# Performance work log

Hardware: AMD Instinct MI355X
Metric: run time of the kernel (lower is better)

## Reference

```python
import jax, jax.numpy as jnp
import numpy as np

D = 300  # feature dim hardcoded in the layer
L = 50   # headline length (e = ones(50))
B = 16384


def setup_inputs() -> dict:
    key = jax.random.key(0)
    ks = jax.random.split(key, 7)
    s = 0.05  # keras initializations.get('normal') uses scale=0.05
    return {
        "Y": jax.random.normal(ks[0], (B, D, L), dtype=jnp.float32),
        "h_n": jax.random.normal(ks[1], (B, D), dtype=jnp.float32),
        "W_y": s * jax.random.normal(ks[2], (D, D), dtype=jnp.float32),
        "W_h": s * jax.random.normal(ks[3], (D, D), dtype=jnp.float32),
        "W_p": s * jax.random.normal(ks[4], (D, D), dtype=jnp.float32),
        "W_x": s * jax.random.normal(ks[5], (D, D), dtype=jnp.float32),
        "w": s * jax.random.normal(ks[6], (D,), dtype=jnp.float32),
    }


def reference(Y, h_n, W_y, W_h, W_p, W_x, w):
    # M = tanh(W_y Y + (W_h h_n) e^T)   -> [B, D, L]
    Wh_h = jnp.einsum('de,be->bd', W_h, h_n)            # [B, D]
    M = jnp.tanh(jnp.einsum('de,bel->bdl', W_y, Y) + Wh_h[:, :, None])
    # alpha = softmax(w^T M) over headline positions    -> [B, L]
    alpha = jax.nn.softmax(jnp.einsum('d,bdl->bl', w, M), axis=-1)
    # r = Y alpha^T                                      -> [B, D]
    r = jnp.einsum('bdl,bl->bd', Y, alpha)
    # h* = tanh(W_p r + W_x h_n)                         -> [B, D]
    h = jnp.tanh(jnp.einsum('de,be->bd', W_p, r) + jnp.einsum('de,be->bd', W_x, h_n))
    return h
```

## Files before the change

kernel.cpp:

```cpp
#include <hip/hip_runtime.h>
#include <hip/hip_bf16.h>

typedef __attribute__((ext_vector_type(8))) short bf16x8;
typedef __attribute__((ext_vector_type(4))) float f32x4;
typedef unsigned short u16;
typedef unsigned int u32;

__device__ __forceinline__ u16 f2bf(float f){
    u32 u; __builtin_memcpy(&u,&f,4);
    u = (u + 0x7FFFu + ((u>>16)&1u)) >> 16;
    return (u16)u;
}
__device__ __forceinline__ float bf2f(u16 h){
    u32 u = ((u32)h)<<16; float f; __builtin_memcpy(&f,&u,4); return f;
}
__device__ __forceinline__ u32 pkbf(float a, float b){
    __hip_bfloat162 h = __float22bfloat162_rn(float2{a,b});
    u32 r; __builtin_memcpy(&r,&h,4); return r;
}
__device__ __forceinline__ float fast_tanh(float x){
    float e = __builtin_amdgcn_exp2f(x * 2.8853900817779268f);
    return 1.f - 2.f*__builtin_amdgcn_rcpf(e + 1.f);
}
__device__ __forceinline__ float wval(const float* W, int d, int e){
    return (d<300 && e<300) ? W[d*300+e] : 0.f;
}

__global__ void k_prep(const float* __restrict__ Wy, const float* __restrict__ Wh,
                       const float* __restrict__ Wp, const float* __restrict__ Wx,
                       const float* __restrict__ w,
                       u16* __restrict__ wy_swz, u16* __restrict__ wh_swz,
                       u16* __restrict__ wpx_swz, float* __restrict__ w_pad)
{
    int gid = blockIdx.x*256 + threadIdx.x;
    if (gid < 320) w_pad[gid] = (gid < 300) ? w[gid] : 0.f;
    u16* dst; const float* A; const float* Bm = nullptr; int t, nks;
    if (gid < 12800)      { dst = wy_swz;  t = gid;        nks = 10; A = Wy; }
    else if (gid < 25600) { dst = wh_swz;  t = gid-12800;  nks = 10; A = Wh; }
    else                  { dst = wpx_swz; t = gid-25600;  nks = 20; A = Wp; Bm = Wx; }
    int ks   = (t/64) % nks;
    int tile = t/(nks*64);
    int lane = t & 63;
    int d  = tile*16 + (lane & 15);
    int kb = ks*32 + (lane>>4)*8;
    u32 pk[4];
    #pragma unroll
    for (int jj=0; jj<4; jj++){
        int k0 = kb + 2*jj, k1 = k0 + 1;
        float v0, v1;
        if (Bm){ v0 = (k0 < 320) ? wval(A,d,k0) : wval(Bm,d,k0-320);
                 v1 = (k1 < 320) ? wval(A,d,k1) : wval(Bm,d,k1-320); }
        else   { v0 = wval(A,d,k0); v1 = wval(A,d,k1); }
        pk[jj] = (u32)f2bf(v0) | ((u32)f2bf(v1) << 16);
    }
    uint4 u; u.x = pk[0]; u.y = pk[1]; u.z = pk[2]; u.w = pk[3];
    ((uint4*)dst)[t] = u;
}

__global__ __launch_bounds__(256,3) void k_whh(const float* __restrict__ hn,
        const u16* __restrict__ wh_swz, u16* __restrict__ whh)
{
    __shared__ __align__(16) u16 A[64*328];
    int tid = threadIdx.x;
    int rb = blockIdx.x >> 1, half = blockIdx.x & 1;
    int m0 = rb*64;
    for (int i = tid; i < 9600; i += 256){
        int r = i/150, c = (i%150)*2;
        float2 v = *(const float2*)(hn + (size_t)(m0+r)*300 + c);
        *(u32*)&A[r*328 + c] = pkbf(v.x, v.y);
    }
    for (int i = tid; i < 64*14; i += 256){ int r = i/14, c = 300 + (i%14)*2; *(u32*)&A[r*328+c] = 0; }
    __syncthreads();
    int w = tid>>6, lane = tid&63, lo = lane&15, hi = lane>>4;
    f32x4 acc[10];
    #pragma unroll
    for (int t=0; t<10; t++) acc[t] = (f32x4){0.f,0.f,0.f,0.f};
    const bf16x8* wsz = (const bf16x8*)wh_swz;
    for (int ks=0; ks<10; ks++){
        bf16x8 aF = *(const bf16x8*)&A[(w*16+lo)*328 + ks*32 + hi*8];
        #pragma unroll
        for (int t=0; t<10; t++){
            int nt = half*10 + t;
            bf16x8 bF = wsz[(nt*10+ks)*64 + lane];
            acc[t] = __builtin_amdgcn_mfma_f32_16x16x32_bf16(aF, bF, acc[t], 0,0,0);
        }
    }
    #pragma unroll
    for (int t=0; t<10; t++)
      #pragma unroll
      for (int rg=0; rg<4; rg++){
        int m = m0 + w*16 + hi*4 + rg;
        whh[(size_t)m*320 + (half*10+t)*16 + lo] = f2bf(acc[t][rg]);
      }
}

__global__ __launch_bounds__(1024) void k_attn(const float* __restrict__ Y,
        const u16* __restrict__ whh, const u16* __restrict__ wy_swz,
        const float* __restrict__ w_pad, u16* __restrict__ r_out)
{
    __shared__ __align__(16) u16 Ylds[50*328];
    __shared__ float whh_s[320];
    __shared__ float w_s[320];
    __shared__ float s_red[8][64];
    __shared__ float alpha_s[64];

    const int tid = threadIdx.x;
    const int wv = tid>>6, lane = tid&63, lo = lane&15, hi = lane>>4;
    const int wd = wv>>1, wc = wv&1;
    const int hi16 = hi*16;
    const int b = blockIdx.x;
    char* Yb8 = (char*)Ylds;
    const float C2L = 2.8853900817779268f;

    int rb_[2];
    { int r0 = (2*wc)*16 + lo;   if (r0>=50) r0-=48; rb_[0]=r0*656;
      int r1 = (2*wc+1)*16 + lo; if (r1>=50) r1-=48; rb_[1]=r1*656; }

    for (int i = tid; i < 320; i += 1024) w_s[i] = w_pad[i];
    for (int i = tid; i < 700; i += 1024){
        int row = i/14, c2 = 150 + i%14;
        *(u32*)(Yb8 + row*656 + c2*4) = 0;
    }
    for (int i = tid; i < 160; i += 1024){
        u32 z = *(const u32*)&whh[(size_t)b*320 + 2*i];
        whh_s[2*i]   = bf2f((u16)(z & 0xffff));
        whh_s[2*i+1] = bf2f((u16)(z >> 16));
    }
    {
        const float* gb_ = Y + (size_t)b*15000;
        #pragma unroll
        for (int it=0; it<4; it++){
            int t = tid + it*1024;
            if (t < 3750){
                int e2 = t/25, l2 = t%25;
                const float* p_ = gb_ + e2*100 + 2*l2;
                float2 sA = *(const float2*)p_;
                float2 sB = *(const float2*)(p_ + 50);
                *(u32*)(Yb8 + (2*l2)*656   + e2*4) = pkbf(sA.x, sB.x);
                *(u32*)(Yb8 + (2*l2+1)*656 + e2*4) = pkbf(sA.y, sB.y);
            }
        }
    }
    __syncthreads();

    const bf16x8* wyf = (const bf16x8*)wy_swz;
    float sp[2] = {0.f,0.f};
    float swd = 0.f;
#define GEMM_BODY(NT)                                                          \
    {                                                                          \
        f32x4 acc[NT][2];                                                      \
        _Pragma("unroll") for (int q=0;q<NT;q++){                              \
            acc[q][0]=(f32x4){0.f,0.f,0.f,0.f};                                \
            acc[q][1]=(f32x4){0.f,0.f,0.f,0.f}; }                              \
        bf16x8 A0[NT], A1[NT], B0[2], B1[2];                                   \
        _Pragma("unroll") for (int q=0;q<NT;q++)                               \
            A0[q] = wyf[((wd+8*q)*10)*64 + lane];                              \
        B0[0] = *(const bf16x8*)(Yb8 + rb_[0] + hi16);                         \
        B0[1] = *(const bf16x8*)(Yb8 + rb_[1] + hi16);                         \
        _Pragma("unroll 1")                                                    \
        for (int kk=0; kk<5; kk++){                                            \
            int k1 = 2*kk+1, k2 = (2*kk+2<10)?(2*kk+2):0;                      \
            _Pragma("unroll") for (int q=0;q<NT;q++)                           \
                A1[q] = wyf[((wd+8*q)*10 + k1)*64 + lane];                     \
            B1[0] = *(const bf16x8*)(Yb8 + rb_[0] + k1*64 + hi16);             \
            B1[1] = *(const bf16x8*)(Yb8 + rb_[1] + k1*64 + hi16);             \
            _Pragma("unroll") for (int q=0;q<NT;q++){                          \
                acc[q][0] = __builtin_amdgcn_mfma_f32_16x16x32_bf16(A0[q],B0[0],acc[q][0],0,0,0); \
                acc[q][1] = __builtin_amdgcn_mfma_f32_16x16x32_bf16(A0[q],B0[1],acc[q][1],0,0,0); } \
            _Pragma("unroll") for (int q=0;q<NT;q++)                           \
                A0[q] = wyf[((wd+8*q)*10 + k2)*64 + lane];                     \
            B0[0] = *(const bf16x8*)(Yb8 + rb_[0] + k2*64 + hi16);             \
            B0[1] = *(const bf16x8*)(Yb8 + rb_[1] + k2*64 + hi16);             \
            _Pragma("unroll") for (int q=0;q<NT;q++){                          \
                acc[q][0] = __builtin_amdgcn_mfma_f32_16x16x32_bf16(A1[q],B1[0],acc[q][0],0,0,0); \
                acc[q][1] = __builtin_amdgcn_mfma_f32_16x16x32_bf16(A1[q],B1[1],acc[q][1],0,0,0); } \
        }                                                                      \
        _Pragma("unroll") for (int q=0;q<NT;q++)                               \
            _Pragma("unroll") for (int rg=0;rg<4;rg++){                        \
                int d = (wd+8*q)*16 + hi*4 + rg;                               \
                float wh = whh_s[d], wd_ = w_s[d];                             \
                float whc = wh*C2L, wd2n = -2.f*wd_;                           \
                swd += wd_;                                                    \
                _Pragma("unroll") for (int c=0;c<2;c++){                       \
                    float targ = __builtin_fmaf(acc[q][c][rg], C2L, whc);      \
                    float e2x  = __builtin_amdgcn_exp2f(targ);                 \
                    float rc   = __builtin_amdgcn_rcpf(e2x + 1.f);             \
                    sp[c] = __builtin_fmaf(wd2n, rc, sp[c]);                   \
                }                                                              \
            }                                                                  \
    }
    if (wd < 3) { GEMM_BODY(3) } else { GEMM_BODY(2) }
#undef GEMM_BODY
    #pragma unroll
    for (int c=0;c<2;c++){
        sp[c] += swd;
        sp[c] += __shfl_xor(sp[c], 16);
        sp[c] += __shfl_xor(sp[c], 32);
    }
    if (lane < 16){
        s_red[wd][(2*wc+0)*16 + lane] = sp[0];
        s_red[wd][(2*wc+1)*16 + lane] = sp[1];
    }
    __syncthreads();

    if (wv == 0){
        float sv = -1e30f;
        if (lane < 50){
            sv = 0.f;
            #pragma unroll
            for (int k=0;k<8;k++) sv += s_red[k][lane];
        }
        float mx = sv;
        #pragma unroll
        for (int off=32; off; off>>=1) mx = fmaxf(mx, __shfl_xor(mx, off));
        float pv = (lane < 50) ? __builtin_amdgcn_exp2f((sv - mx)*1.4426950408889634f) : 0.f;
        float sm = pv;
        #pragma unroll
        for (int off=32; off; off>>=1) sm += __shfl_xor(sm, off);
        alpha_s[lane] = pv * __builtin_amdgcn_rcpf(sm);
    }
    __syncthreads();

    if (tid < 160){
        float r0 = 0.f, r1 = 0.f;
        if (tid < 150){
            #pragma unroll 10
            for (int l=0; l<50; l++){
                u32 z = *(const u32*)(Yb8 + l*656 + tid*4);
                float a_ = alpha_s[l];
                r0 = __builtin_fmaf(a_, bf2f((u16)(z & 0xffff)), r0);
                r1 = __builtin_fmaf(a_, bf2f((u16)(z >> 16)),   r1);
            }
        }
        *(u32*)&r_out[(size_t)b*320 + 2*tid] = pkbf(r0, r1);
    }
}

__global__ __launch_bounds__(256,3) void k_out(const u16* __restrict__ r_in,
        const float* __restrict__ hn, const u16* __restrict__ wpx_swz,
        float* __restrict__ out)
{
    __shared__ __align__(16) u16 A[32*648];
    int tid = threadIdx.x;
    int m0 = blockIdx.x*32;
    for (int i = tid; i < 32*40; i += 256){
        int r = i/40, c8 = (i%40)*8;
        uint4 v = *(const uint4*)&r_in[(size_t)(m0+r)*320 + c8];
        *(uint4*)&A[r*648 + c8] = v;
    }
    for (int i = tid; i < 32*150; i += 256){
        int r = i/150, c = (i%150)*2;
        float2 v = *(const float2*)(hn + (size_t)(m0+r)*300 + c);
        *(u32*)&A[r*648 + 320 + c] = pkbf(v.x, v.y);
    }
    for (int i = tid; i < 32*14; i += 256){ int r = i/14, c = 620 + (i%14)*2; *(u32*)&A[r*648+c] = 0; }
    __syncthreads();
    int w = tid>>6, lane = tid&63, lo = lane&15, hi = lane>>4;
    int wm = w & 1, wn = w >> 1;
    f32x4 acc[10];
    #pragma unroll
    for (int t=0; t<10; t++) acc[t] = (f32x4){0.f,0.f,0.f,0.f};
    const bf16x8* wsz = (const bf16x8*)wpx_swz;
    for (int ks=0; ks<20; ks++){
        bf16x8 aF = *(const bf16x8*)&A[(wm*16+lo)*648 + ks*32 + hi*8];
        #pragma unroll
        for (int t=0; t<10; t++){
            int nt = wn*10 + t;
            bf16x8 bF = wsz[(nt*20+ks)*64 + lane];
            acc[t] = __builtin_amdgcn_mfma_f32_16x16x32_bf16(aF, bF, acc[t], 0,0,0);
        }
    }
    #pragma unroll
    for (int t=0; t<10; t++){
        int n = (wn*10+t)*16 + lo;
        if (n < 300){
            #pragma unroll
            for (int rg=0; rg<4; rg++){
                int m = m0 + wm*16 + hi*4 + rg;
                out[(size_t)m*300 + n] = fast_tanh(acc[t][rg]);
            }
        }
    }
}

extern "C" void kernel_launch(void* const* d_in, const int* in_sizes, int n_in,
                              void* d_out, int out_size, void* d_ws, size_t ws_size,
                              hipStream_t stream)
{
    const float* Y  = (const float*)d_in[0];
    const float* hn = (const float*)d_in[1];
    const float* Wy = (const float*)d_in[2];
    const float* Wh = (const float*)d_in[3];
    const float* Wp = (const float*)d_in[4];
    const float* Wx = (const float*)d_in[5];
    const float* w  = (const float*)d_in[6];
    int B = in_sizes[1] / 300;

    char* ws = (char*)d_ws;
    u16*   wy_swz  = (u16*)(ws + 0);
    u16*   wh_swz  = (u16*)(ws + 204800);
    u16*   wpx_swz = (u16*)(ws + 409600);
    float* w_pad   = (float*)(ws + 819200);
    u16*   whh     = (u16*)(ws + 820480);
    u16*   r_ws    = (u16*)(ws + 820480 + (size_t)B*640);

    k_prep<<<200, 256, 0, stream>>>(Wy, Wh, Wp, Wx, w, wy_swz, wh_swz, wpx_swz, w_pad);
    k_whh <<<(B/64)*2, 256, 0, stream>>>(hn, wh_swz, whh);
    k_attn<<<B, 1024, 0, stream>>>(Y, whh, wy_swz, w_pad, r_ws);
    k_out <<<B/32, 256, 0, stream>>>(r_ws, hn, wpx_swz, (float*)d_out);
}
```

Measured before the change: 485.6 us.

## Process two batch rows per attention block to reuse W_y fragments

Each k_attn block now handles two batch elements, stacking their Y tiles into one 100-column LDS buffer (stride reduced to 624 bytes). The column tiles are split 4/3 across wave pairs, so each W_y fragment loaded from global is reused across up to four MFMA column tiles instead of two. This halves the grid size and W_y fetch traffic per sample. In exchange it needs about 70KB of dynamic LDS, which may lower blocks per CU and makes the work uneven between wave pairs.

```diff
diff --git a/kernel.cpp b/kernel.cpp
--- a/kernel.cpp
+++ b/kernel.cpp
@@ -94,121 +94,146 @@
       }
 }
 
+#define YSTR 624
+#define OFF_SRED  62432
+#define OFF_ALPHA (62432+3584)
+#define OFF_WHH   (62432+3584+512)
+#define OFF_WS    (62432+3584+512+2560)
+#define DYN_LDS   70400
+
 __global__ __launch_bounds__(1024) void k_attn(const float* __restrict__ Y,
         const u16* __restrict__ whh, const u16* __restrict__ wy_swz,
         const float* __restrict__ w_pad, u16* __restrict__ r_out)
 {
-    __shared__ __align__(16) u16 Ylds[50*328];
-    __shared__ float whh_s[320];
-    __shared__ float w_s[320];
-    __shared__ float s_red[8][64];
-    __shared__ float alpha_s[64];
+    extern __shared__ __align__(16) char smem[];
+    char*  Yb8     = smem;
+    float (*s_red)[112] = (float(*)[112])(smem + OFF_SRED);
+    float (*alpha_s)[64]= (float(*)[64]) (smem + OFF_ALPHA);
+    float (*whh_s)[320] = (float(*)[320])(smem + OFF_WHH);
+    float* w_s          = (float*)       (smem + OFF_WS);
 
     const int tid = threadIdx.x;
     const int wv = tid>>6, lane = tid&63, lo = lane&15, hi = lane>>4;
     const int wd = wv>>1, wc = wv&1;
     const int hi16 = hi*16;
-    const int b = blockIdx.x;
-    char* Yb8 = (char*)Ylds;
+    const int b0 = blockIdx.x*2;
     const float C2L = 2.8853900817779268f;
 
-    int rb_[2];
-    { int r0 = (2*wc)*16 + lo;   if (r0>=50) r0-=48; rb_[0]=r0*656;
-      int r1 = (2*wc+1)*16 + lo; if (r1>=50) r1-=48; rb_[1]=r1*656; }
+    const int NCT = wc ? 3 : 4;
+    const int CB  = wc ? 4 : 0;
+    int rb_[4];
+    #pragma unroll
+    for (int c=0;c<4;c++){
+        int row = (CB + (c<NCT?c:0))*16 + lo;
+        if (row >= 100) row -= 48;
+        rb_[c] = row*YSTR;
+    }
 
     for (int i = tid; i < 320; i += 1024) w_s[i] = w_pad[i];
-    for (int i = tid; i < 700; i += 1024){
-        int row = i/14, c2 = 150 + i%14;
-        *(u32*)(Yb8 + row*656 + c2*4) = 0;
-    }
-    for (int i = tid; i < 160; i += 1024){
-        u32 z = *(const u32*)&whh[(size_t)b*320 + 2*i];
-        whh_s[2*i]   = bf2f((u16)(z & 0xffff));
-        whh_s[2*i+1] = bf2f((u16)(z >> 16));
+    for (int i = tid; i < 608; i += 1024){
+        if (i < 600){ int row = i/6, c2 = 150 + i%6;
+                      *(u32*)(Yb8 + row*YSTR + c2*4) = 0; }
+        else        { *(u32*)(Yb8 + 62400 + (i-600)*4) = 0; }
+    }
+    for (int i = tid; i < 320; i += 1024){
+        int bb = i/160, k = i%160;
+        u32 z = *(const u32*)&whh[(size_t)(b0+bb)*320 + 2*k];
+        whh_s[bb][2*k]   = bf2f((u16)(z & 0xffff));
+        whh_s[bb][2*k+1] = bf2f((u16)(z >> 16));
     }
     {
-        const float* gb_ = Y + (size_t)b*15000;
-        #pragma unroll
-        for (int it=0; it<4; it++){
+        const float* gb_ = Y + (size_t)b0*15000;
+        #pragma unroll
+        for (int it=0; it<8; it++){
             int t = tid + it*1024;
-            if (t < 3750){
-                int e2 = t/25, l2 = t%25;
-                const float* p_ = gb_ + e2*100 + 2*l2;
+            if (t < 7500){
+                int bb = t/3750, tt = t%3750;
+                int e2 = tt/25, l2 = tt%25;
+                const float* p_ = gb_ + bb*15000 + e2*100 + 2*l2;
                 float2 sA = *(const float2*)p_;
                 float2 sB = *(const float2*)(p_ + 50);
-                *(u32*)(Yb8 + (2*l2)*656   + e2*4) = pkbf(sA.x, sB.x);
-                *(u32*)(Yb8 + (2*l2+1)*656 + e2*4) = pkbf(sA.y, sB.y);
+                int r0 = bb*50 + 2*l2;
+                *(u32*)(Yb8 + r0*YSTR        + e2*4) = pkbf(sA.x, sB.x);
+                *(u32*)(Yb8 + (r0+1)*YSTR    + e2*4) = pkbf(sA.y, sB.y);
             }
         }
     }
     __syncthreads();
 
     const bf16x8* wyf = (const bf16x8*)wy_swz;
-    float sp[2] = {0.f,0.f};
+    float sp[4] = {0.f,0.f,0.f,0.f};
     float swd = 0.f;
 #define GEMM_BODY(NT)                                                          \
     {                                                                          \
-        f32x4 acc[NT][2];                                                      \
-        _Pragma("unroll") for (int q=0;q<NT;q++){                              \
-            acc[q][0]=(f32x4){0.f,0.f,0.f,0.f};                                \
-            acc[q][1]=(f32x4){0.f,0.f,0.f,0.f}; }                              \
-        bf16x8 A0[NT], A1[NT], B0[2], B1[2];                                   \
+        f32x4 acc[NT][4];                                                      \
+        _Pragma("unroll") for (int q=0;q<NT;q++)                               \
+            _Pragma("unroll") for (int c=0;c<4;c++)                            \
+                acc[q][c] = (f32x4){0.f,0.f,0.f,0.f};                          \
+        bf16x8 A0[NT], A1[NT], B[4];                                           \
         _Pragma("unroll") for (int q=0;q<NT;q++)                               \
             A0[q] = wyf[((wd+8*q)*10)*64 + lane];                              \
-        B0[0] = *(const bf16x8*)(Yb8 + rb_[0] + hi16);                         \
-        B0[1] = *(const bf16x8*)(Yb8 + rb_[1] + hi16);                         \
         _Pragma("unroll 1")                                                    \
         for (int kk=0; kk<5; kk++){                                            \
-            int k1 = 2*kk+1, k2 = (2*kk+2<10)?(2*kk+2):0;                      \
+            int k0 = 2*kk, k1 = 2*kk+1, k2 = (2*kk+2<10)?(2*kk+2):0;           \
             _Pragma("unroll") for (int q=0;q<NT;q++)                           \
                 A1[q] = wyf[((wd+8*q)*10 + k1)*64 + lane];                     \
-            B1[0] = *(const bf16x8*)(Yb8 + rb_[0] + k1*64 + hi16);             \
-            B1[1] = *(const bf16x8*)(Yb8 + rb_[1] + k1*64 + hi16);             \
-            _Pragma("unroll") for (int q=0;q<NT;q++){                          \
-                acc[q][0] = __builtin_amdgcn_mfma_f32_16x16x32_bf16(A0[q],B0[0],acc[q][0],0,0,0); \
-                acc[q][1] = __builtin_amdgcn_mfma_f32_16x16x32_bf16(A0[q],B0[1],acc[q][1],0,0,0); } \
+            _Pragma("unroll") for (int c=0;c<4;c++)                            \
+                if (c < NCT) B[c] = *(const bf16x8*)(Yb8 + rb_[c] + k0*64 + hi16); \
+            _Pragma("unroll") for (int q=0;q<NT;q++)                           \
+                _Pragma("unroll") for (int c=0;c<4;c++)                        \
+                    if (c < NCT)                                               \
+                        acc[q][c] = __builtin_amdgcn_mfma_f32_16x16x32_bf16(   \
+                            A0[q], B[c], acc[q][c], 0,0,0);                    \
             _Pragma("unroll") for (int q=0;q<NT;q++)                           \
                 A0[q] = wyf[((wd+8*q)*10 + k2)*64 + lane];                     \
-            B0[0] = *(const bf16x8*)(Yb8 + rb_[0] + k2*64 + hi16);             \
-            B0[1] = *(const bf16x8*)(Yb8 + rb_[1] + k2*64 + hi16);             \
-            _Pragma("unroll") for (int q=0;q<NT;q++){                          \
-                acc[q][0] = __builtin_amdgcn_mfma_f32_16x16x32_bf16(A1[q],B1[0],acc[q][0],0,0,0); \
-                acc[q][1] = __builtin_amdgcn_mfma_f32_16x16x32_bf16(A1[q],B1[1],acc[q][1],0,0,0); } \
+            _Pragma("unroll") for (int c=0;c<4;c++)                            \
+                if (c < NCT) B[c] = *(const bf16x8*)(Yb8 + rb_[c] + k1*64 + hi16); \
+            _Pragma("unroll") for (int q=0;q<NT;q++)                           \
+                _Pragma("unroll") for (int c=0;c<4;c++)                        \
+                    if (c < NCT)                                               \
+                        acc[q][c] = __builtin_amdgcn_mfma_f32_16x16x32_bf16(   \
+                            A1[q], B[c], acc[q][c], 0,0,0);                    \
         }                                                                      \
         _Pragma("unroll") for (int q=0;q<NT;q++)                               \
             _Pragma("unroll") for (int rg=0;rg<4;rg++){                        \
                 int d = (wd+8*q)*16 + hi*4 + rg;                               \
-                float wh = whh_s[d], wd_ = w_s[d];                             \
-                float whc = wh*C2L, wd2n = -2.f*wd_;                           \
+                float wh0 = whh_s[0][d], wh1 = whh_s[1][d], wd_ = w_s[d];      \
+                float wd2n = -2.f*wd_;                                         \
                 swd += wd_;                                                    \
-                _Pragma("unroll") for (int c=0;c<2;c++){                       \
-                    float targ = __builtin_fmaf(acc[q][c][rg], C2L, whc);      \
-                    float e2x  = __builtin_amdgcn_exp2f(targ);                 \
-                    float rc   = __builtin_amdgcn_rcpf(e2x + 1.f);             \
-                    sp[c] = __builtin_fmaf(wd2n, rc, sp[c]);                   \
+                _Pragma("unroll") for (int c=0;c<4;c++){                       \
+                    if (c < NCT){                                              \
+                        int col = (CB+c)*16 + lo;                              \
+                        float wh = (col < 50) ? wh0 : wh1;                     \
+                        float targ = (acc[q][c][rg] + wh) * C2L;               \
+                        float e2x  = __builtin_amdgcn_exp2f(targ);             \
+                        float rc   = __builtin_amdgcn_rcpf(e2x + 1.f);         \
+                        sp[c] = __builtin_fmaf(wd2n, rc, sp[c]);               \
+                    }                                                          \
                 }                                                              \
             }                                                                  \
     }
     if (wd < 3) { GEMM_BODY(3) } else { GEMM_BODY(2) }
 #undef GEMM_BODY
     #pragma unroll
-    for (int c=0;c<2;c++){
+    for (int c=0;c<4;c++){
         sp[c] += swd;
         sp[c] += __shfl_xor(sp[c], 16);
         sp[c] += __shfl_xor(sp[c], 32);
     }
     if (lane < 16){
-        s_red[wd][(2*wc+0)*16 + lane] = sp[0];
-        s_red[wd][(2*wc+1)*16 + lane] = sp[1];
-    }
-    __syncthreads();
-
-    if (wv == 0){
+        #pragma unroll
+        for (int c=0;c<4;c++)
+            if (c < NCT) s_red[wd][(CB+c)*16 + lane] = sp[c];
+    }
+    __syncthreads();
+
+    if (wv < 2){
+        int bb = wv;
         float sv = -1e30f;
         if (lane < 50){
             sv = 0.f;
             #pragma unroll
-            for (int k=0;k<8;k++) sv += s_red[k][lane];
+            for (int k=0;k<8;k++) sv += s_red[k][bb*50 + lane];
         }
         float mx = sv;
         #pragma unroll
@@ -217,22 +242,24 @@
         float sm = pv;
         #pragma unroll
         for (int off=32; off; off>>=1) sm += __shfl_xor(sm, off);
-        alpha_s[lane] = pv * __builtin_amdgcn_rcpf(sm);
-    }
-    __syncthreads();
-
-    if (tid < 160){
+        alpha_s[bb][lane] = pv * __builtin_amdgcn_rcpf(sm);
+    }
+    __syncthreads();
+
+    if (tid < 320){
+        int bb = tid/160, i = tid%160;
         float r0 = 0.f, r1 = 0.f;
-        if (tid < 150){
+        if (i < 150){
+            const char* base = Yb8 + bb*50*YSTR + i*4;
             #pragma unroll 10
             for (int l=0; l<50; l++){
-                u32 z = *(const u32*)(Yb8 + l*656 + tid*4);
-                float a_ = alpha_s[l];
+                u32 z = *(const u32*)(base + l*YSTR);
+                float a_ = alpha_s[bb][l];
                 r0 = __builtin_fmaf(a_, bf2f((u16)(z & 0xffff)), r0);
                 r1 = __builtin_fmaf(a_, bf2f((u16)(z >> 16)),   r1);
             }
         }
-        *(u32*)&r_out[(size_t)b*320 + 2*tid] = pkbf(r0, r1);
+        *(u32*)&r_out[(size_t)(b0+bb)*320 + 2*i] = pkbf(r0, r1);
     }
 }
 
@@ -304,8 +331,11 @@
     u16*   whh     = (u16*)(ws + 820480);
     u16*   r_ws    = (u16*)(ws + 820480 + (size_t)B*640);
 
+    (void)hipFuncSetAttribute((const void*)k_attn,
+            hipFuncAttributeMaxDynamicSharedMemorySize, DYN_LDS);
+
     k_prep<<<200, 256, 0, stream>>>(Wy, Wh, Wp, Wx, w, wy_swz, wh_swz, wpx_swz, w_pad);
     k_whh <<<(B/64)*2, 256, 0, stream>>>(hn, wh_swz, whh);
-    k_attn<<<B, 1024, 0, stream>>>(Y, whh, wy_swz, w_pad, r_ws);
+    k_attn<<<B/2, 1024, DYN_LDS, stream>>>(Y, whh, wy_swz, w_pad, r_ws);
     k_out <<<B/32, 256, 0, stream>>>(r_ws, hn, wpx_swz, (float*)d_out);
 }
```

Result: slower. 509.1 us (+4.8%).
